# Kernel tuning notes

Hardware: AMD Instinct MI355X
Metric: run time of the kernel (lower is better)

The kernel has to match this reference:

```python
import jax, jax.numpy as jnp
import numpy as np

S = 14
L_COORD = 5.0
L_NOOBJ = 0.5


def setup_inputs() -> dict:
    key = jax.random.key(0)
    k1, k2, k3, k4 = jax.random.split(key, 4)
    N = 4096
    # positive uniforms so sqrt(w), sqrt(h) and IoU areas are well-defined (as in real YOLO outputs)
    pred_tensor = jax.random.uniform(k1, (N, S, S, 30), dtype=jnp.float32, minval=0.01, maxval=1.0)
    target_boxes = jax.random.uniform(k2, (N, S, S, 4), dtype=jnp.float32, minval=0.01, maxval=1.0)
    target_cls = jax.random.uniform(k3, (N, S, S, 20), dtype=jnp.float32)
    has_object_map = jax.random.bernoulli(k4, 0.15, (N, S, S))
    return {"pred_tensor": pred_tensor, "target_boxes": target_boxes,
            "target_cls": target_cls, "has_object_map": has_object_map}


def _xywh2xyxy(b):
    # b: (..., 4) as [cx, cy, w, h]; cx,cy are in grid units -> divide by S
    x, y, w, h = b[..., 0], b[..., 1], b[..., 2], b[..., 3]
    return jnp.stack([x / S - 0.5 * w, y / S - 0.5 * h,
                      x / S + 0.5 * w, y / S + 0.5 * h], axis=-1)


def _iou_pairwise(b1, b2):
    # elementwise IoU between matched boxes (diag of compute_iou), b: (..., 4) xyxy
    lt = jnp.maximum(b1[..., :2], b2[..., :2])
    rb = jnp.minimum(b1[..., 2:], b2[..., 2:])
    wh = jnp.maximum(rb - lt, 0.0)
    inter = wh[..., 0] * wh[..., 1]
    a1 = (b1[..., 2] - b1[..., 0]) * (b1[..., 3] - b1[..., 1])
    a2 = (b2[..., 2] - b2[..., 0]) * (b2[..., 3] - b2[..., 1])
    return inter / (a1 + a2 - inter)


def reference(pred_tensor, target_boxes, target_cls, has_object_map):
    N = pred_tensor.shape[0]
    obj = has_object_map.astype(pred_tensor.dtype)          # (N,S,S)
    noobj = 1.0 - obj

    box1 = pred_tensor[..., 0:5]
    box2 = pred_tensor[..., 5:10]
    pred_cls = pred_tensor[..., 10:]

    # class loss: masked sum-MSE over object cells
    cls_loss = jnp.sum(obj[..., None] * (pred_cls - target_cls) ** 2)

    # no-object loss: confidences of both predictors in non-object cells vs 0
    no_obj_loss = L_NOOBJ * jnp.sum(noobj * (box1[..., 4] ** 2 + box2[..., 4] ** 2))

    # best-of-B selection by IoU against target (elementwise, matched per cell)
    tgt_xyxy = _xywh2xyxy(target_boxes)
    iou1 = _iou_pairwise(_xywh2xyxy(box1[..., :4]), tgt_xyxy)
    iou2 = _iou_pairwise(_xywh2xyxy(box2[..., :4]), tgt_xyxy)
    take1 = iou1 > iou2
    best_iou = jnp.where(take1, iou1, iou2)                  # (N,S,S)
    best_box = jnp.where(take1[..., None], box1, box2)       # (N,S,S,5)

    xy_err = jnp.sum((best_box[..., :2] - target_boxes[..., :2]) ** 2, axis=-1)
    wh_err = jnp.sum((jnp.sqrt(best_box[..., 2:4]) - jnp.sqrt(target_boxes[..., 2:4])) ** 2, axis=-1)
    reg_loss = L_COORD * jnp.sum(obj * (xy_err + wh_err))

    # containing-object confidence loss; target IoU is detached
    contain_loss = jnp.sum(obj * (best_box[..., 4] - jax.lax.stop_gradient(best_iou)) ** 2)

    total = cls_loss + no_obj_loss + contain_loss + reg_loss
    # [total, reg, containing_obj, no_obj, cls], each averaged over batch
    return jnp.stack([total, reg_loss, contain_loss, no_obj_loss, cls_loss]) / N
```

## Files before the change

### kernel.cpp

```cpp
#include <hip/hip_runtime.h>


#define NBATCH   4096
#define CELLS    (NBATCH * 14 * 14)
#define THREADS  256
#define NBLK     2048
#define NWAVES   (NBLK * 4)
#define CHUNKS   (CELLS / 32)
#define L_COORD  5.0f
#define L_NOOBJ  0.5f

__global__ __launch_bounds__(THREADS, 8) void yolo_main(
    const float* __restrict__ pred,
    const float* __restrict__ tbox,
    const float* __restrict__ tcls,
    const int*   __restrict__ objmap,
    float4*      __restrict__ part)
{
    __shared__ float lds[4 * 960];
    __shared__ float red[4][4];

    const int tid  = threadIdx.x;
    const int wv   = tid >> 6;
    const int lane = tid & 63;
    float* seg = &lds[wv * 960];
    float4* s4 = (float4*)seg;

    const int i1  = lane + 64, i2 = lane + 128;
    const int cc0 = lane / 5;
    const int cc1 = i1 / 5;
    const int cc2 = (lane < 32) ? (i2 / 5) : 0;
    const int ch0a = (lane - cc0 * 5) * 4;
    const int ch0b = (i1   - cc1 * 5) * 4;
    const int ch0c = (i2   - cc2 * 5) * 4;
    const int bcell = lane >> 1;
    const int box   = lane & 1;
    const int l31   = lane & 31;
    const float invS = 1.0f / 14.0f;

    float acc_reg = 0.f, acc_cont = 0.f, acc_noobj = 0.f, acc_cls = 0.f;

    const int gw0 = blockIdx.x * 4 + wv;

    float4 pv0, pv1, pv2, pv3;
    float4 tbv;
    int    ov;
    {
        const size_t cb = (size_t)gw0 * 32;
        const float4* p4 = (const float4*)pred + (size_t)gw0 * 240;
        ov  = objmap[cb + l31];
        tbv = ((const float4*)tbox)[cb + bcell];
        pv0 = p4[lane];
        pv1 = p4[i1];
        pv2 = p4[i2];
        if (lane < 48) pv3 = p4[lane + 192];
    }

    for (int c = gw0; c < CHUNKS; c += NWAVES) {
        float4 a0 = pv0, a1 = pv1, a2 = pv2, a3 = pv3;
        float4 tb = tbv;
        int    ob = ov;

        const int cn = c + NWAVES;
        if (cn < CHUNKS) {
            const size_t cb = (size_t)cn * 32;
            const float4* p4 = (const float4*)pred + (size_t)cn * 240;
            ov  = objmap[cb + l31];
            tbv = ((const float4*)tbox)[cb + bcell];
            pv0 = p4[lane];
            pv1 = p4[i1];
            pv2 = p4[i2];
            if (lane < 48) pv3 = p4[lane + 192];
        }

        s4[lane] = a0;
        s4[i1]   = a1;
        s4[i2]   = a2;
        if (lane < 48) s4[lane + 192] = a3;

        const int o0  = __shfl(ob, cc0);
        const int o1  = __shfl(ob, cc1);
        const int o2  = __shfl(ob, cc2);
        const int obx = __shfl(ob, bcell);

        float4 t0, t1, t2;
        const float4* t4 = (const float4*)tcls + (size_t)c * 160;
        const bool g0 = (o0 != 0);
        const bool g1 = (o1 != 0);
        const bool g2 = (lane < 32) && (o2 != 0);
        if (g0) t0 = t4[lane];
        if (g1) t1 = t4[i1];
        if (g2) t2 = t4[i2];

        {
            const float* pp = &seg[bcell * 30 + box * 5];
            float x = pp[0], y = pp[1], w = pp[2], h = pp[3], conf = pp[4];

            if (!obx) acc_noobj += conf * conf;

            float txc = tb.x * invS, tyc = tb.y * invS;
            float tx1 = txc - 0.5f * tb.z, ty1 = tyc - 0.5f * tb.w;
            float tx2 = txc + 0.5f * tb.z, ty2 = tyc + 0.5f * tb.w;
            float ta  = (tx2 - tx1) * (ty2 - ty1);

            float ax1 = x * invS - 0.5f * w, ay1 = y * invS - 0.5f * h;
            float ax2 = x * invS + 0.5f * w, ay2 = y * invS + 0.5f * h;
            float a1b = (ax2 - ax1) * (ay2 - ay1);
            float iw  = fmaxf(fminf(ax2, tx2) - fmaxf(ax1, tx1), 0.f);
            float ih  = fmaxf(fminf(ay2, ty2) - fmaxf(ay1, ty1), 0.f);
            float inter = iw * ih;
            float iou   = inter / (a1b + ta - inter);

            float iou_other = __shfl_xor(iou, 1);
            bool win = (box == 0) ? (iou > iou_other) : !(iou_other > iou);

            if (win && obx) {
                float dx = x - tb.x, dy = y - tb.y;
                float dw = sqrtf(w) - sqrtf(tb.z);
                float dh = sqrtf(h) - sqrtf(tb.w);
                acc_reg  += dx*dx + dy*dy + dw*dw + dh*dh;
                float dc  = conf - iou;
                acc_cont += dc * dc;
            }
        }

        {
            float cl = 0.f;
            if (g0) {
                const float* pc = &seg[cc0 * 30 + 10 + ch0a];
                float d0 = pc[0]-t0.x, d1 = pc[1]-t0.y, d2 = pc[2]-t0.z, d3 = pc[3]-t0.w;
                cl += d0*d0 + d1*d1 + d2*d2 + d3*d3;
            }
            if (g1) {
                const float* pc = &seg[cc1 * 30 + 10 + ch0b];
                float d0 = pc[0]-t1.x, d1 = pc[1]-t1.y, d2 = pc[2]-t1.z, d3 = pc[3]-t1.w;
                cl += d0*d0 + d1*d1 + d2*d2 + d3*d3;
            }
            if (g2) {
                const float* pc = &seg[cc2 * 30 + 10 + ch0c];
                float d0 = pc[0]-t2.x, d1 = pc[1]-t2.y, d2 = pc[2]-t2.z, d3 = pc[3]-t2.w;
                cl += d0*d0 + d1*d1 + d2*d2 + d3*d3;
            }
            acc_cls += cl;
        }
    }

    #pragma unroll
    for (int off = 32; off > 0; off >>= 1) {
        acc_reg   += __shfl_down(acc_reg,   off);
        acc_cont  += __shfl_down(acc_cont,  off);
        acc_noobj += __shfl_down(acc_noobj, off);
        acc_cls   += __shfl_down(acc_cls,   off);
    }
    if (lane == 0) {
        red[wv][0] = acc_reg;
        red[wv][1] = acc_cont;
        red[wv][2] = acc_noobj;
        red[wv][3] = acc_cls;
    }
    __syncthreads();
    if (tid == 0) {
        float4 p;
        p.x = red[0][0] + red[1][0] + red[2][0] + red[3][0];
        p.y = red[0][1] + red[1][1] + red[2][1] + red[3][1];
        p.z = red[0][2] + red[1][2] + red[2][2] + red[3][2];
        p.w = red[0][3] + red[1][3] + red[2][3] + red[3][3];
        part[blockIdx.x] = p;
    }
}

__global__ __launch_bounds__(1024) void yolo_reduce(
    const float4* __restrict__ part, float* __restrict__ out)
{
    __shared__ float red[16][4];
    float r = 0.f, c = 0.f, n = 0.f, cl = 0.f;
    #pragma unroll
    for (int i = threadIdx.x; i < NBLK; i += 1024) {
        float4 p = part[i];
        r += p.x; c += p.y; n += p.z; cl += p.w;
    }
    #pragma unroll
    for (int off = 32; off > 0; off >>= 1) {
        r  += __shfl_down(r,  off);
        c  += __shfl_down(c,  off);
        n  += __shfl_down(n,  off);
        cl += __shfl_down(cl, off);
    }
    const int wave = threadIdx.x >> 6, lane = threadIdx.x & 63;
    if (lane == 0) {
        red[wave][0] = r; red[wave][1] = c; red[wave][2] = n; red[wave][3] = cl;
    }
    __syncthreads();
    if (threadIdx.x == 0) {
        float R = 0.f, C = 0.f, Nn = 0.f, Cl = 0.f;
        #pragma unroll
        for (int w = 0; w < 16; ++w) {
            R += red[w][0]; C += red[w][1]; Nn += red[w][2]; Cl += red[w][3];
        }
        const float invN = 1.0f / (float)NBATCH;
        float reg   = L_COORD * R  * invN;
        float cont  =           C  * invN;
        float noobj = L_NOOBJ * Nn * invN;
        float cls   =           Cl * invN;
        out[0] = reg + cont + noobj + cls;
        out[1] = reg;
        out[2] = cont;
        out[3] = noobj;
        out[4] = cls;
    }
}

extern "C" void kernel_launch(void* const* d_in, const int* in_sizes, int n_in,
                              void* d_out, int out_size, void* d_ws, size_t ws_size,
                              hipStream_t stream) {
    const float* pred   = (const float*)d_in[0];
    const float* tbox   = (const float*)d_in[1];
    const float* tcls   = (const float*)d_in[2];
    const int*   objmap = (const int*)  d_in[3];
    float4* part = (float4*)d_ws;
    float*  out  = (float*)d_out;

    yolo_main<<<NBLK, THREADS, 0, stream>>>(pred, tbox, tcls, objmap, part);
    yolo_reduce<<<1, 1024, 0, stream>>>(part, out);
}
```

Baseline: 222.5 us.

## Skip loading class predictions and target boxes for non-object cells

Float4 loads of pred that fall entirely inside the class region of a cell without an object are redirected to the chunk's first element. The same is done for the target boxes of non-object cells, so less DRAM traffic is needed at the 15% object rate. The register prefetch of the next chunk's pred and tbox is dropped, and only the object map is prefetched one iteration ahead. Redirected lanes still issue loads (to a shared cached address), and losing the prefetch exposes more memory latency per iteration.

```diff
diff --git a/kernel.cpp b/kernel.cpp
--- a/kernel.cpp
+++ b/kernel.cpp
@@ -25,6 +25,14 @@
     const int lane = tid & 63;
     float* seg = &lds[wv * 960];
     float4* s4 = (float4*)seg;
+
+    const int jA = lane, jB = lane + 64, jC = lane + 128, jD = lane + 192;
+    #define SKC(j)  ((((4*(j)) / 30) == ((4*(j)+3) / 30)) && (((4*(j)) % 30) >= 10))
+    #define CELL(j) ((4*(j)) / 30)
+    const bool skAc = SKC(jA); const int cA = CELL(jA);
+    const bool skBc = SKC(jB); const int cB = CELL(jB);
+    const bool skCc = SKC(jC); const int cC = CELL(jC);
+    const bool skDc = SKC(jD); const int cD = (jD < 240) ? CELL(jD) : 0;
 
     const int i1  = lane + 64, i2 = lane + 128;
     const int cc0 = lane / 5;
@@ -42,55 +50,45 @@
 
     const int gw0 = blockIdx.x * 4 + wv;
 
-    float4 pv0, pv1, pv2, pv3;
-    float4 tbv;
-    int    ov;
-    {
-        const size_t cb = (size_t)gw0 * 32;
-        const float4* p4 = (const float4*)pred + (size_t)gw0 * 240;
-        ov  = objmap[cb + l31];
-        tbv = ((const float4*)tbox)[cb + bcell];
-        pv0 = p4[lane];
-        pv1 = p4[i1];
-        pv2 = p4[i2];
-        if (lane < 48) pv3 = p4[lane + 192];
-    }
+    int ov = (gw0 < CHUNKS) ? objmap[(size_t)gw0 * 32 + l31] : 0;
 
     for (int c = gw0; c < CHUNKS; c += NWAVES) {
-        float4 a0 = pv0, a1 = pv1, a2 = pv2, a3 = pv3;
-        float4 tb = tbv;
-        int    ob = ov;
-
-        const int cn = c + NWAVES;
-        if (cn < CHUNKS) {
-            const size_t cb = (size_t)cn * 32;
-            const float4* p4 = (const float4*)pred + (size_t)cn * 240;
-            ov  = objmap[cb + l31];
-            tbv = ((const float4*)tbox)[cb + bcell];
-            pv0 = p4[lane];
-            pv1 = p4[i1];
-            pv2 = p4[i2];
-            if (lane < 48) pv3 = p4[lane + 192];
-        }
-
-        s4[lane] = a0;
-        s4[i1]   = a1;
-        s4[i2]   = a2;
-        if (lane < 48) s4[lane + 192] = a3;
+        const int ob = ov;
 
         const int o0  = __shfl(ob, cc0);
         const int o1  = __shfl(ob, cc1);
         const int o2  = __shfl(ob, cc2);
         const int obx = __shfl(ob, bcell);
-
-        float4 t0, t1, t2;
-        const float4* t4 = (const float4*)tcls + (size_t)c * 160;
+        const bool skA = skAc && (__shfl(ob, cA) == 0);
+        const bool skB = skBc && (__shfl(ob, cB) == 0);
+        const bool skC = skCc && (__shfl(ob, cC) == 0);
+        const bool skD = skDc && (__shfl(ob, cD) == 0);
+        const bool gb = (obx != 0);
         const bool g0 = (o0 != 0);
         const bool g1 = (o1 != 0);
         const bool g2 = (lane < 32) && (o2 != 0);
-        if (g0) t0 = t4[lane];
-        if (g1) t1 = t4[i1];
-        if (g2) t2 = t4[i2];
+
+        const float4* p4 = (const float4*)pred + (size_t)c * 240;
+        float4 aA = p4[skA ? 0 : jA];
+        float4 aB = p4[skB ? 0 : jB];
+        float4 aC = p4[skC ? 0 : jC];
+        float4 aD;
+        if (lane < 48) aD = p4[skD ? 0 : jD];
+
+        const int cn = c + NWAVES;
+        if (cn < CHUNKS) ov = objmap[(size_t)cn * 32 + l31];
+
+        const size_t cb4 = (size_t)c * 32;
+        float4 tb = ((const float4*)tbox)[cb4 + (gb ? bcell : 0)];
+        const float4* t4 = (const float4*)tcls + (size_t)c * 160;
+        float4 t0 = t4[g0 ? lane : 0];
+        float4 t1 = t4[g1 ? i1   : 0];
+        float4 t2 = t4[g2 ? i2   : 0];
+
+        s4[jA] = aA;
+        s4[jB] = aB;
+        s4[jC] = aC;
+        if (lane < 48) s4[jD] = aD;
 
         {
             const float* pp = &seg[bcell * 30 + box * 5];
```

Measured after the change: 208.8 us. 1.07x faster.
